# Kernel tuning notes

Hardware: AMD Instinct MI355X
Metric: run time of the kernel (lower is better)

The kernel has to match this reference:

```python
import jax, jax.numpy as jnp
import numpy as np

N_NODES = 50000
N_EDGES = 500000
IN_CH = 128
HID = 64
HEADS = 4
N_LAYERS = 3
OUT_CH = 16
N_GRAPHS = 64
NEG_SLOPE = 0.2  # PyG GATConv default


def setup_inputs() -> dict:
    key = jax.random.key(0)
    ks = jax.random.split(key, 20)
    inp = {
        'x': jax.random.normal(ks[0], (N_NODES, IN_CH), dtype=jnp.float32),
        'edge_attr': jax.random.normal(ks[1], (N_EDGES, 8), dtype=jnp.float32),
        'edge_index': jax.random.randint(ks[2], (2, N_EDGES), 0, N_NODES, dtype=jnp.int64),
        'batch': jnp.sort(jax.random.randint(ks[3], (N_NODES,), 0, N_GRAPHS, dtype=jnp.int64)),
    }
    kidx = 4
    in_dim = IN_CH
    for i in range(N_LAYERS):
        inp[f'W{i}'] = jax.random.normal(ks[kidx], (in_dim, HEADS * HID), dtype=jnp.float32) * (1.0 / np.sqrt(in_dim)); kidx += 1
        inp[f'asrc{i}'] = jax.random.normal(ks[kidx], (HEADS, HID), dtype=jnp.float32) * 0.1; kidx += 1
        inp[f'adst{i}'] = jax.random.normal(ks[kidx], (HEADS, HID), dtype=jnp.float32) * 0.1; kidx += 1
        inp[f'b{i}'] = jnp.zeros((HEADS * HID,), dtype=jnp.float32)
        in_dim = HEADS * HID
    inp['Wc'] = jax.random.normal(ks[kidx], (HEADS * HID, OUT_CH), dtype=jnp.float32) * (1.0 / np.sqrt(HEADS * HID)); kidx += 1
    inp['bc'] = jnp.zeros((OUT_CH,), dtype=jnp.float32)
    return inp


def _gat_layer(x, src, dst, W, asrc, adst, b):
    # x: [N, F_in] -> h: [N, H, C]
    N = x.shape[0]
    h = (x @ W).reshape(N, HEADS, HID)
    s_src = jnp.einsum('nhc,hc->nh', h, asrc)  # [N, H]
    s_dst = jnp.einsum('nhc,hc->nh', h, adst)
    e = jax.nn.leaky_relu(s_src[src] + s_dst[dst], NEG_SLOPE)  # [E, H]
    # segment softmax over incoming edges of each destination node
    m = jax.ops.segment_max(e, dst, num_segments=N)            # [N, H]
    ex = jnp.exp(e - m[dst])
    denom = jax.ops.segment_sum(ex, dst, num_segments=N)       # [N, H]
    alpha = ex / (denom[dst] + 1e-16)                           # [E, H]
    out = jax.ops.segment_sum(alpha[:, :, None] * h[src], dst, num_segments=N)  # [N, H, C]
    return out.reshape(N, HEADS * HID) + b


def reference(x, edge_attr, edge_index, batch,
              W0, asrc0, adst0, b0,
              W1, asrc1, adst1, b1,
              W2, asrc2, adst2, b2,
              Wc, bc):
    N = x.shape[0]
    loop = jnp.arange(N, dtype=edge_index.dtype)
    # PyG GATConv adds self-loops by default
    src = jnp.concatenate([edge_index[0], loop])
    dst = jnp.concatenate([edge_index[1], loop])
    params = [(W0, asrc0, adst0, b0), (W1, asrc1, adst1, b1), (W2, asrc2, adst2, b2)]
    h = x
    for (W, asrc, adst, b) in params:
        h = jax.nn.relu(_gat_layer(h, src, dst, W, asrc, adst, b))
        # nn.Dropout(0.5) is identity in eval mode
    pooled = jax.ops.segment_sum(h, batch, num_segments=N_GRAPHS)  # global_add_pool
    return pooled @ Wc + bc
```

## Files before the change

kernel.cpp:

```cpp
#include <hip/hip_runtime.h>
#include <hip/hip_bf16.h>

#define NNODES 50000
#define NEDGES 500000
#define INCH 128
#define HID 64
#define HEADS 4
#define FDIM 256
#define NGRAPHS 64
#define OUTCH 16
#define NEG_SLOPE 0.2f

#define BM 64
#define BN 256
#define BK 32

typedef float f32x4 __attribute__((ext_vector_type(4)));
typedef __bf16 bf16x8 __attribute__((ext_vector_type(8)));

__device__ inline unsigned short f2bf_rne(float x) {
    unsigned int u = __float_as_uint(x);
    unsigned int r = (u + 0x7FFFu + ((u >> 16) & 1u)) >> 16;
    return (unsigned short)r;
}
__device__ inline float bf2f(unsigned short s) {
    return __uint_as_float(((unsigned int)s) << 16);
}
__device__ inline void split2(float x, unsigned short& h, unsigned short& l) {
    h = f2bf_rne(x);
    float hf = __uint_as_float(((unsigned int)h) << 16);
    l = f2bf_rne(x - hf);
}
__device__ inline void gld_lds16(const void* g, void* l) {
    __builtin_amdgcn_global_load_lds((__attribute__((address_space(1))) void*)g,
                                     (__attribute__((address_space(3))) void*)l, 16, 0, 0);
}


__global__ void k_hist(const int* __restrict__ dst, int E, int* __restrict__ counts) {
    int i = blockIdx.x * blockDim.x + threadIdx.x;
    if (i < E) atomicAdd(&counts[dst[i]], 1);
}

__global__ __launch_bounds__(256) void k_blocksum(const int* __restrict__ counts, int N,
                                                  int* __restrict__ bsum) {
    int idx = blockIdx.x * 256 + threadIdx.x;
    int v = (idx < N) ? counts[idx] : 0;
#pragma unroll
    for (int off = 32; off; off >>= 1) v += __shfl_xor(v, off);
    __shared__ int wsum[4];
    if ((threadIdx.x & 63) == 0) wsum[threadIdx.x >> 6] = v;
    __syncthreads();
    if (threadIdx.x == 0) bsum[blockIdx.x] = wsum[0] + wsum[1] + wsum[2] + wsum[3];
}

__global__ __launch_bounds__(256) void k_scanfinal(const int* __restrict__ counts,
                                                   const int* __restrict__ bsum, int N,
                                                   int* __restrict__ rowstart) {
    __shared__ int tmp[256];
    __shared__ int wsum[4];
    int t = threadIdx.x, b = blockIdx.x;
    int p = 0;
    for (int i = t; i < b; i += 256) p += bsum[i];
#pragma unroll
    for (int off = 32; off; off >>= 1) p += __shfl_xor(p, off);
    int idx = b * 256 + t;
    int v = (idx < N) ? counts[idx] : 0;
    tmp[t] = v;
    if ((t & 63) == 0) wsum[t >> 6] = p;
    __syncthreads();
    int bp = wsum[0] + wsum[1] + wsum[2] + wsum[3];
    for (int off = 1; off < 256; off <<= 1) {
        int u = (t >= off) ? tmp[t - off] : 0;
        __syncthreads();
        tmp[t] += u;
        __syncthreads();
    }
    if (idx < N) rowstart[idx + 1] = bp + tmp[t];
    if (idx == 0) rowstart[0] = 0;
}

__global__ void k_scatter(const int* __restrict__ src, const int* __restrict__ dst, int E,
                          const int* __restrict__ rowstart, int* __restrict__ cursor,
                          int* __restrict__ csr_src) {
    int i = blockIdx.x * blockDim.x + threadIdx.x;
    if (i < E) {
        int d = dst[i];
        int p = atomicAdd(&cursor[d], 1);
        csr_src[rowstart[d] + p] = src[i];
    }
}


__global__ void k_wdecomp(const float* __restrict__ W, unsigned short* __restrict__ Wth,
                          unsigned short* __restrict__ Wtl, int K) {
    int i = blockIdx.x * 256 + threadIdx.x;
    if (i >= K * 256) return;
    int k = i >> 8, n = i & 255;
    unsigned short h, l;
    split2(W[i], h, l);
    Wth[n * K + k] = h;
    Wtl[n * K + k] = l;
}


__global__ void k_adecomp(const float* __restrict__ X, unsigned short* __restrict__ Xh,
                          unsigned short* __restrict__ Xl, int total4) {
    int i = blockIdx.x * 256 + threadIdx.x;
    if (i >= total4) return;
    float4 v = ((const float4*)X)[i];
    ushort4 h, l;
    split2(v.x, h.x, l.x);
    split2(v.y, h.y, l.y);
    split2(v.z, h.z, l.z);
    split2(v.w, h.w, l.w);
    ((ushort4*)Xh)[i] = h;
    ((ushort4*)Xl)[i] = l;
}


__global__ __launch_bounds__(256) void k_gemm_mfma(
    const unsigned short* __restrict__ Aph, const unsigned short* __restrict__ Apl,
    const unsigned short* __restrict__ Bph, const unsigned short* __restrict__ Bpl,
    const float* __restrict__ av, const float* __restrict__ dv,
    unsigned short* __restrict__ Hb16,
    float* __restrict__ ssrcO, float* __restrict__ sdstO, int M, int K) {
    __shared__ unsigned short sAh[BM * BK];
    __shared__ unsigned short sAl[BM * BK];
    __shared__ unsigned short sBh[BN * BK];
    __shared__ unsigned short sBl[BN * BK];

    const int t = threadIdx.x;
    const int row0 = blockIdx.x * BM;
    const int wv = t >> 6, ln = t & 63, lr = ln & 15, lk = ln >> 4;

    const int ar = wv * 16 + (ln >> 2);
    const int alc = (ln & 3) ^ ((ar >> 1) & 3);
    const size_t agoff = (size_t)min(row0 + ar, M - 1) * K + alc * 8;
    const int fsc = lk ^ ((lr >> 1) & 3);

    f32x4 acc[4][4] = {};

    for (int k0 = 0; k0 < K; k0 += BK) {
        gld_lds16(Aph + agoff + k0, &sAh[wv * 512]);
        gld_lds16(Apl + agoff + k0, &sAl[wv * 512]);
#pragma unroll
        for (int j = 0; j < 4; ++j) {
            int br = j * 64 + wv * 16 + (ln >> 2);
            int blc = (ln & 3) ^ ((br >> 1) & 3);
            size_t go = (size_t)br * K + k0 + blc * 8;
            gld_lds16(Bph + go, &sBh[j * 2048 + wv * 512]);
            gld_lds16(Bpl + go, &sBl[j * 2048 + wv * 512]);
        }
        __syncthreads();

        bf16x8 ah[4], al[4];
#pragma unroll
        for (int mi = 0; mi < 4; ++mi) {
            int r = mi * 16 + lr;
            ah[mi] = *(const bf16x8*)&sAh[r * 32 + fsc * 8];
            al[mi] = *(const bf16x8*)&sAl[r * 32 + fsc * 8];
        }
#pragma unroll
        for (int ni = 0; ni < 4; ++ni) {
            int br = wv * 64 + ni * 16 + lr;
            bf16x8 bh = *(const bf16x8*)&sBh[br * 32 + fsc * 8];
            bf16x8 bl = *(const bf16x8*)&sBl[br * 32 + fsc * 8];
#pragma unroll
            for (int mi = 0; mi < 4; ++mi) {
                acc[mi][ni] = __builtin_amdgcn_mfma_f32_16x16x32_bf16(ah[mi], bh, acc[mi][ni], 0, 0, 0);
                acc[mi][ni] = __builtin_amdgcn_mfma_f32_16x16x32_bf16(ah[mi], bl, acc[mi][ni], 0, 0, 0);
                acc[mi][ni] = __builtin_amdgcn_mfma_f32_16x16x32_bf16(al[mi], bh, acc[mi][ni], 0, 0, 0);
            }
        }
        __syncthreads();
    }

    float ps[4][4] = {}, pd[4][4] = {};
#pragma unroll
    for (int ni = 0; ni < 4; ++ni) {
        int col = wv * 64 + ni * 16 + lr;
        float a_s = av[col], a_d = dv[col];
#pragma unroll
        for (int mi = 0; mi < 4; ++mi) {
            f32x4 v = acc[mi][ni];
            int r = row0 + mi * 16 + lk * 4;
#pragma unroll
            for (int j = 0; j < 4; ++j) {
                if (r + j < M) Hb16[(size_t)(r + j) * FDIM + col] = f2bf_rne(v[j]);
                ps[mi][j] += v[j] * a_s;
                pd[mi][j] += v[j] * a_d;
            }
        }
    }
#pragma unroll
    for (int mi = 0; mi < 4; ++mi) {
#pragma unroll
        for (int j = 0; j < 4; ++j) {
            float s = ps[mi][j], q = pd[mi][j];
            s += __shfl_xor(s, 1); s += __shfl_xor(s, 2);
            s += __shfl_xor(s, 4); s += __shfl_xor(s, 8);
            q += __shfl_xor(q, 1); q += __shfl_xor(q, 2);
            q += __shfl_xor(q, 4); q += __shfl_xor(q, 8);
            if (lr == 0) {
                int r = row0 + mi * 16 + lk * 4 + j;
                if (r < M) {
                    ssrcO[r * HEADS + wv] = s;
                    sdstO[r * HEADS + wv] = q;
                }
            }
        }
    }
}


__global__ __launch_bounds__(256) void k_aggregate(
    const unsigned short* __restrict__ hb,
    const float* __restrict__ ssrc, const float* __restrict__ sdst,
    const int* __restrict__ rowstart, const int* __restrict__ csr_src,
    const float* __restrict__ bias,
    unsigned short* __restrict__ oh, unsigned short* __restrict__ ol, int N) {
    int wv = threadIdx.x >> 6, ln = threadIdx.x & 63;
    int n = blockIdx.x * 4 + wv;
    if (n >= N) return;
    int head = ln >> 4;
    int fo = head * 64 + (ln & 15) * 4;
    float sd = sdst[n * HEADS + head];
    float e = ssrc[n * HEADS + head] + sd;
    e = (e > 0.f) ? e : NEG_SLOPE * e;
    float m = e, d = 1.0f;
    ushort4 sv = *(const ushort4*)&hb[(size_t)n * FDIM + fo];
    float4 acc = make_float4(bf2f(sv.x), bf2f(sv.y), bf2f(sv.z), bf2f(sv.w));
    int r0 = rowstart[n], r1 = rowstart[n + 1];
    int r = r0;
    for (; r + 3 < r1; r += 4) {
        int s0 = csr_src[r], s1 = csr_src[r + 1], s2 = csr_src[r + 2], s3 = csr_src[r + 3];
        ushort4 u0 = *(const ushort4*)&hb[(size_t)s0 * FDIM + fo];
        ushort4 u1 = *(const ushort4*)&hb[(size_t)s1 * FDIM + fo];
        ushort4 u2 = *(const ushort4*)&hb[(size_t)s2 * FDIM + fo];
        ushort4 u3 = *(const ushort4*)&hb[(size_t)s3 * FDIM + fo];
        float c0 = ssrc[s0 * HEADS + head] + sd;
        float c1 = ssrc[s1 * HEADS + head] + sd;
        float c2 = ssrc[s2 * HEADS + head] + sd;
        float c3 = ssrc[s3 * HEADS + head] + sd;
        c0 = (c0 > 0.f) ? c0 : NEG_SLOPE * c0;
        c1 = (c1 > 0.f) ? c1 : NEG_SLOPE * c1;
        c2 = (c2 > 0.f) ? c2 : NEG_SLOPE * c2;
        c3 = (c3 > 0.f) ? c3 : NEG_SLOPE * c3;
        float mn = fmaxf(m, fmaxf(fmaxf(c0, c1), fmaxf(c2, c3)));
        float wa = __expf(m - mn);
        float w0 = __expf(c0 - mn), w1 = __expf(c1 - mn);
        float w2 = __expf(c2 - mn), w3 = __expf(c3 - mn);
        acc.x = acc.x * wa + bf2f(u0.x) * w0 + bf2f(u1.x) * w1 + bf2f(u2.x) * w2 + bf2f(u3.x) * w3;
        acc.y = acc.y * wa + bf2f(u0.y) * w0 + bf2f(u1.y) * w1 + bf2f(u2.y) * w2 + bf2f(u3.y) * w3;
        acc.z = acc.z * wa + bf2f(u0.z) * w0 + bf2f(u1.z) * w1 + bf2f(u2.z) * w2 + bf2f(u3.z) * w3;
        acc.w = acc.w * wa + bf2f(u0.w) * w0 + bf2f(u1.w) * w1 + bf2f(u2.w) * w2 + bf2f(u3.w) * w3;
        d = d * wa + ((w0 + w1) + (w2 + w3));
        m = mn;
    }
    for (; r < r1; ++r) {
        int s0 = csr_src[r];
        float sc = ssrc[s0 * HEADS + head] + sd;
        sc = (sc > 0.f) ? sc : NEG_SLOPE * sc;
        ushort4 u0 = *(const ushort4*)&hb[(size_t)s0 * FDIM + fo];
        float mn = fmaxf(m, sc);
        float wa = __expf(m - mn), wn = __expf(sc - mn);
        acc.x = acc.x * wa + bf2f(u0.x) * wn;
        acc.y = acc.y * wa + bf2f(u0.y) * wn;
        acc.z = acc.z * wa + bf2f(u0.z) * wn;
        acc.w = acc.w * wa + bf2f(u0.w) * wn;
        d = d * wa + wn;
        m = mn;
    }
    float inv = 1.0f / d;
    float4 bv = *(const float4*)&bias[fo];
    float o0 = fmaxf(acc.x * inv + bv.x, 0.f);
    float o1 = fmaxf(acc.y * inv + bv.y, 0.f);
    float o2 = fmaxf(acc.z * inv + bv.z, 0.f);
    float o3 = fmaxf(acc.w * inv + bv.w, 0.f);
    ushort4 hh, ll;
    split2(o0, hh.x, ll.x);
    split2(o1, hh.y, ll.y);
    split2(o2, hh.z, ll.z);
    split2(o3, hh.w, ll.w);
    *(ushort4*)&oh[(size_t)n * FDIM + fo] = hh;
    *(ushort4*)&ol[(size_t)n * FDIM + fo] = ll;
}


__global__ __launch_bounds__(256) void k_pool(const unsigned short* __restrict__ oh,
                                              const unsigned short* __restrict__ ol,
                                              const int* __restrict__ batch,
                                              float* __restrict__ pooled, int N) {
    int f = threadIdx.x;
    int n0 = blockIdx.x * 128;
    if (n0 >= N) return;
    int n1 = min(n0 + 128, N);
    int g = batch[n0];
    float run = 0.f;
    for (int n = n0; n < n1; ++n) {
        int gn = batch[n];
        if (gn != g) {
            atomicAdd(&pooled[g * FDIM + f], run);
            run = 0.f;
            g = gn;
        }
        run += bf2f(oh[(size_t)n * FDIM + f]) + bf2f(ol[(size_t)n * FDIM + f]);
    }
    atomicAdd(&pooled[g * FDIM + f], run);
}


__global__ __launch_bounds__(256) void k_final(const float* __restrict__ pooled,
                                               const float* __restrict__ Wc,
                                               const float* __restrict__ bc,
                                               float* __restrict__ out) {
    int tid = blockIdx.x * 256 + threadIdx.x;
    int g = tid >> 4, o = tid & 15;
    float s = bc[o];
    for (int k = 0; k < FDIM; ++k) s += pooled[g * FDIM + k] * Wc[k * OUTCH + o];
    out[g * OUTCH + o] = s;
}


extern "C" void kernel_launch(void* const* d_in, const int* in_sizes, int n_in,
                              void* d_out, int out_size, void* d_ws, size_t ws_size,
                              hipStream_t stream) {
    const float* x = (const float*)d_in[0];
    const int* edge_index = (const int*)d_in[2];
    const int* batch = (const int*)d_in[3];
    const float* W[3]    = {(const float*)d_in[4], (const float*)d_in[8],  (const float*)d_in[12]};
    const float* asrc[3] = {(const float*)d_in[5], (const float*)d_in[9],  (const float*)d_in[13]};
    const float* adst[3] = {(const float*)d_in[6], (const float*)d_in[10], (const float*)d_in[14]};
    const float* bias[3] = {(const float*)d_in[7], (const float*)d_in[11], (const float*)d_in[15]};
    const float* Wc = (const float*)d_in[16];
    const float* bc = (const float*)d_in[17];

    const int N = in_sizes[3];
    const int E = in_sizes[2] / 2;
    const int* e_src = edge_index;
    const int* e_dst = edge_index + E;

    char* ws = (char*)d_ws;
    size_t off = 0;
    unsigned short* hb = (unsigned short*)(ws + off); off += (size_t)N * FDIM * 2;
    unsigned short* xh = (unsigned short*)(ws + off); off += (size_t)N * INCH * 2;
    unsigned short* xl = (unsigned short*)(ws + off); off += (size_t)N * INCH * 2;
    unsigned short* P0h = (unsigned short*)(ws + off); off += (size_t)N * FDIM * 2;
    unsigned short* P0l = (unsigned short*)(ws + off); off += (size_t)N * FDIM * 2;
    unsigned short* P1h = (unsigned short*)(ws + off); off += (size_t)N * FDIM * 2;
    unsigned short* P1l = (unsigned short*)(ws + off); off += (size_t)N * FDIM * 2;
    float* ssrc = (float*)(ws + off); off += (size_t)N * HEADS * 4;
    float* sdst = (float*)(ws + off); off += (size_t)N * HEADS * 4;
    int* rowstart = (int*)(ws + off); off += ((size_t)(N + 1) * 4 + 255) / 256 * 256;
    int* cursor = (int*)(ws + off); off += (size_t)N * 4;
    int* csr_src = (int*)(ws + off); off += (size_t)E * 4;
    float* pooled = (float*)(ws + off); off += (size_t)NGRAPHS * FDIM * 4;
    int* bsum = (int*)(ws + off); off += ((size_t)((N + 255) / 256) * 4 + 255) / 256 * 256;
    unsigned short* Wth[3];
    unsigned short* Wtl[3];
    int Ks[3] = {INCH, FDIM, FDIM};
    for (int l = 0; l < 3; ++l) {
        Wth[l] = (unsigned short*)(ws + off); off += (size_t)256 * Ks[l] * 2;
        Wtl[l] = (unsigned short*)(ws + off); off += (size_t)256 * Ks[l] * 2;
    }

    const int nb = (N + 255) / 256;

    hipMemsetAsync(cursor, 0, (size_t)N * 4, stream);
    k_hist<<<(E + 255) / 256, 256, 0, stream>>>(e_dst, E, cursor);
    k_blocksum<<<nb, 256, 0, stream>>>(cursor, N, bsum);
    k_scanfinal<<<nb, 256, 0, stream>>>(cursor, bsum, N, rowstart);
    hipMemsetAsync(cursor, 0, (size_t)N * 4, stream);
    k_scatter<<<(E + 255) / 256, 256, 0, stream>>>(e_src, e_dst, E, rowstart, cursor, csr_src);

    k_adecomp<<<((N * INCH / 4) + 255) / 256, 256, 0, stream>>>(x, xh, xl, N * INCH / 4);
    for (int l = 0; l < 3; ++l)
        k_wdecomp<<<(Ks[l] * 256 + 255) / 256, 256, 0, stream>>>(W[l], Wth[l], Wtl[l], Ks[l]);

    const unsigned short* Ah = xh;
    const unsigned short* Al = xl;
    unsigned short* Oh[3] = {P0h, P1h, P0h};
    unsigned short* Ol[3] = {P0l, P1l, P0l};
    for (int l = 0; l < 3; ++l) {
        int K = Ks[l];
        k_gemm_mfma<<<(N + BM - 1) / BM, 256, 0, stream>>>(Ah, Al, Wth[l], Wtl[l], asrc[l],
                                                           adst[l], hb, ssrc, sdst, N, K);
        k_aggregate<<<(N + 3) / 4, 256, 0, stream>>>(hb, ssrc, sdst, rowstart, csr_src,
                                                     bias[l], Oh[l], Ol[l], N);
        Ah = Oh[l];
        Al = Ol[l];
    }

    hipMemsetAsync(pooled, 0, (size_t)NGRAPHS * FDIM * 4, stream);
    k_pool<<<(N + 127) / 128, 256, 0, stream>>>(P0h, P0l, batch, pooled, N);
    k_final<<<4, 256, 0, stream>>>(pooled, Wc, bc, (float*)d_out);
}
```

Before: 393.7 us.

## Switch split-bf16 GEMM to single fp16, double-buffer LDS, batch aggregation

Replaces the three-MFMA split-bf16 (hi/lo) emulation of fp32 GEMM with a single fp16 MFMA per tile, and stores activations as one fp16 tensor instead of hi/lo pairs. This cuts GEMM compute and activation memory traffic. The GEMM also gets double-buffered LDS staging, the aggregation loop processes neighbours in batches of 8 with clamped indices, and the CSR build folds the cursor init into the scan to drop one memset. The trade-off is lower precision (fp16 range and mantissa) compared with the near-fp32 split scheme.

```diff
diff --git a/kernel.cpp b/kernel.cpp
--- a/kernel.cpp
+++ b/kernel.cpp
@@ -16,21 +16,9 @@
 #define BK 32
 
 typedef float f32x4 __attribute__((ext_vector_type(4)));
-typedef __bf16 bf16x8 __attribute__((ext_vector_type(8)));
-
-__device__ inline unsigned short f2bf_rne(float x) {
-    unsigned int u = __float_as_uint(x);
-    unsigned int r = (u + 0x7FFFu + ((u >> 16) & 1u)) >> 16;
-    return (unsigned short)r;
-}
-__device__ inline float bf2f(unsigned short s) {
-    return __uint_as_float(((unsigned int)s) << 16);
-}
-__device__ inline void split2(float x, unsigned short& h, unsigned short& l) {
-    h = f2bf_rne(x);
-    float hf = __uint_as_float(((unsigned int)h) << 16);
-    l = f2bf_rne(x - hf);
-}
+typedef _Float16 f16x8 __attribute__((ext_vector_type(8)));
+typedef _Float16 f16x4 __attribute__((ext_vector_type(4)));
+
 __device__ inline void gld_lds16(const void* g, void* l) {
     __builtin_amdgcn_global_load_lds((__attribute__((address_space(1))) void*)g,
                                      (__attribute__((address_space(3))) void*)l, 16, 0, 0);
@@ -56,7 +44,8 @@
 
 __global__ __launch_bounds__(256) void k_scanfinal(const int* __restrict__ counts,
                                                    const int* __restrict__ bsum, int N,
-                                                   int* __restrict__ rowstart) {
+                                                   int* __restrict__ rowstart,
+                                                   int* __restrict__ cursor) {
     __shared__ int tmp[256];
     __shared__ int wsum[4];
     int t = threadIdx.x, b = blockIdx.x;
@@ -76,59 +65,48 @@
         tmp[t] += u;
         __syncthreads();
     }
-    if (idx < N) rowstart[idx + 1] = bp + tmp[t];
+    if (idx < N) {
+        int incl = bp + tmp[t];
+        rowstart[idx + 1] = incl;
+        cursor[idx] = incl - v;
+    }
     if (idx == 0) rowstart[0] = 0;
 }
 
 __global__ void k_scatter(const int* __restrict__ src, const int* __restrict__ dst, int E,
-                          const int* __restrict__ rowstart, int* __restrict__ cursor,
-                          int* __restrict__ csr_src) {
+                          int* __restrict__ cursor, int* __restrict__ csr_src) {
     int i = blockIdx.x * blockDim.x + threadIdx.x;
     if (i < E) {
-        int d = dst[i];
-        int p = atomicAdd(&cursor[d], 1);
-        csr_src[rowstart[d] + p] = src[i];
-    }
-}
-
-
-__global__ void k_wdecomp(const float* __restrict__ W, unsigned short* __restrict__ Wth,
-                          unsigned short* __restrict__ Wtl, int K) {
+        int p = atomicAdd(&cursor[dst[i]], 1);
+        csr_src[p] = src[i];
+    }
+}
+
+
+__global__ void k_wdecomp(const float* __restrict__ W, _Float16* __restrict__ Wt, int K) {
     int i = blockIdx.x * 256 + threadIdx.x;
     if (i >= K * 256) return;
     int k = i >> 8, n = i & 255;
-    unsigned short h, l;
-    split2(W[i], h, l);
-    Wth[n * K + k] = h;
-    Wtl[n * K + k] = l;
-}
-
-
-__global__ void k_adecomp(const float* __restrict__ X, unsigned short* __restrict__ Xh,
-                          unsigned short* __restrict__ Xl, int total4) {
+    Wt[n * K + k] = (_Float16)W[i];
+}
+
+
+__global__ void k_adecomp(const float* __restrict__ X, _Float16* __restrict__ Xf, int total4) {
     int i = blockIdx.x * 256 + threadIdx.x;
     if (i >= total4) return;
     float4 v = ((const float4*)X)[i];
-    ushort4 h, l;
-    split2(v.x, h.x, l.x);
-    split2(v.y, h.y, l.y);
-    split2(v.z, h.z, l.z);
-    split2(v.w, h.w, l.w);
-    ((ushort4*)Xh)[i] = h;
-    ((ushort4*)Xl)[i] = l;
+    f16x4 o = {(_Float16)v.x, (_Float16)v.y, (_Float16)v.z, (_Float16)v.w};
+    ((f16x4*)Xf)[i] = o;
 }
 
 
 __global__ __launch_bounds__(256) void k_gemm_mfma(
-    const unsigned short* __restrict__ Aph, const unsigned short* __restrict__ Apl,
-    const unsigned short* __restrict__ Bph, const unsigned short* __restrict__ Bpl,
+    const _Float16* __restrict__ A, const _Float16* __restrict__ B,
     const float* __restrict__ av, const float* __restrict__ dv,
-    unsigned short* __restrict__ Hb16,
+    _Float16* __restrict__ Hf,
     float* __restrict__ ssrcO, float* __restrict__ sdstO, int M, int K) {
-    __shared__ unsigned short sAh[BM * BK];
-    __shared__ unsigned short sAl[BM * BK];
-    __shared__ unsigned short sBh[BN * BK];
-    __shared__ unsigned short sBl[BN * BK];
+    __shared__ _Float16 sA[2][BM * BK];
+    __shared__ _Float16 sB[2][BN * BK];
 
     const int t = threadIdx.x;
     const int row0 = blockIdx.x * BM;
@@ -137,44 +115,44 @@
     const int ar = wv * 16 + (ln >> 2);
     const int alc = (ln & 3) ^ ((ar >> 1) & 3);
     const size_t agoff = (size_t)min(row0 + ar, M - 1) * K + alc * 8;
+    const int brr = wv * 16 + (ln >> 2);
     const int fsc = lk ^ ((lr >> 1) & 3);
 
     f32x4 acc[4][4] = {};
-
-    for (int k0 = 0; k0 < K; k0 += BK) {
-        gld_lds16(Aph + agoff + k0, &sAh[wv * 512]);
-        gld_lds16(Apl + agoff + k0, &sAl[wv * 512]);
-#pragma unroll
-        for (int j = 0; j < 4; ++j) {
-            int br = j * 64 + wv * 16 + (ln >> 2);
-            int blc = (ln & 3) ^ ((br >> 1) & 3);
-            size_t go = (size_t)br * K + k0 + blc * 8;
-            gld_lds16(Bph + go, &sBh[j * 2048 + wv * 512]);
-            gld_lds16(Bpl + go, &sBl[j * 2048 + wv * 512]);
+    const int nt = K / BK;
+
+#define STAGE(tt, p)                                                        \
+    do {                                                                    \
+        int _k0 = (tt)*BK;                                                  \
+        gld_lds16(A + agoff + _k0, &sA[p][wv * 512]);                       \
+        _Pragma("unroll") for (int _j = 0; _j < 4; ++_j) {                  \
+            int _br = _j * 64 + brr;                                        \
+            int _blc = (ln & 3) ^ ((_br >> 1) & 3);                         \
+            gld_lds16(B + (size_t)_br * K + _k0 + _blc * 8,                 \
+                      &sB[p][_j * 2048 + wv * 512]);                        \
+        }                                                                   \
+    } while (0)
+
+    STAGE(0, 0);
+    __syncthreads();
+    for (int tt = 0; tt < nt; ++tt) {
+        int cur = tt & 1;
+        if (tt + 1 < nt) STAGE(tt + 1, cur ^ 1);
+
+        f16x8 af[4];
+#pragma unroll
+        for (int mi = 0; mi < 4; ++mi)
+            af[mi] = *(const f16x8*)&sA[cur][(mi * 16 + lr) * BK + fsc * 8];
+#pragma unroll
+        for (int ni = 0; ni < 4; ++ni) {
+            f16x8 bf = *(const f16x8*)&sB[cur][(wv * 64 + ni * 16 + lr) * BK + fsc * 8];
+#pragma unroll
+            for (int mi = 0; mi < 4; ++mi)
+                acc[mi][ni] = __builtin_amdgcn_mfma_f32_16x16x32_f16(af[mi], bf, acc[mi][ni], 0, 0, 0);
         }
         __syncthreads();
-
-        bf16x8 ah[4], al[4];
-#pragma unroll
-        for (int mi = 0; mi < 4; ++mi) {
-            int r = mi * 16 + lr;
-            ah[mi] = *(const bf16x8*)&sAh[r * 32 + fsc * 8];
-            al[mi] = *(const bf16x8*)&sAl[r * 32 + fsc * 8];
-        }
-#pragma unroll
-        for (int ni = 0; ni < 4; ++ni) {
-            int br = wv * 64 + ni * 16 + lr;
-            bf16x8 bh = *(const bf16x8*)&sBh[br * 32 + fsc * 8];
-            bf16x8 bl = *(const bf16x8*)&sBl[br * 32 + fsc * 8];
-#pragma unroll
-            for (int mi = 0; mi < 4; ++mi) {
-                acc[mi][ni] = __builtin_amdgcn_mfma_f32_16x16x32_bf16(ah[mi], bh, acc[mi][ni], 0, 0, 0);
-                acc[mi][ni] = __builtin_amdgcn_mfma_f32_16x16x32_bf16(ah[mi], bl, acc[mi][ni], 0, 0, 0);
-                acc[mi][ni] = __builtin_amdgcn_mfma_f32_16x16x32_bf16(al[mi], bh, acc[mi][ni], 0, 0, 0);
-            }
-        }
-        __syncthreads();
-    }
+    }
+#undef STAGE
 
     float ps[4][4] = {}, pd[4][4] = {};
 #pragma unroll
@@ -187,7 +165,7 @@
             int r = row0 + mi * 16 + lk * 4;
 #pragma unroll
             for (int j = 0; j < 4; ++j) {
-                if (r + j < M) Hb16[(size_t)(r + j) * FDIM + col] = f2bf_rne(v[j]);
+                if (r + j < M) Hf[(size_t)(r + j) * FDIM + col] = (_Float16)v[j];
                 ps[mi][j] += v[j] * a_s;
                 pd[mi][j] += v[j] * a_d;
             }
@@ -215,11 +193,11 @@
 
 
 __global__ __launch_bounds__(256) void k_aggregate(
-    const unsigned short* __restrict__ hb,
+    const _Float16* __restrict__ hf,
     const float* __restrict__ ssrc, const float* __restrict__ sdst,
     const int* __restrict__ rowstart, const int* __restrict__ csr_src,
     const float* __restrict__ bias,
-    unsigned short* __restrict__ oh, unsigned short* __restrict__ ol, int N) {
+    _Float16* __restrict__ outf, int N) {
     int wv = threadIdx.x >> 6, ln = threadIdx.x & 63;
     int n = blockIdx.x * 4 + wv;
     if (n >= N) return;
@@ -229,67 +207,58 @@
     float e = ssrc[n * HEADS + head] + sd;
     e = (e > 0.f) ? e : NEG_SLOPE * e;
     float m = e, d = 1.0f;
-    ushort4 sv = *(const ushort4*)&hb[(size_t)n * FDIM + fo];
-    float4 acc = make_float4(bf2f(sv.x), bf2f(sv.y), bf2f(sv.z), bf2f(sv.w));
+    f16x4 sv = *(const f16x4*)&hf[(size_t)n * FDIM + fo];
+    float4 acc = make_float4((float)sv[0], (float)sv[1], (float)sv[2], (float)sv[3]);
     int r0 = rowstart[n], r1 = rowstart[n + 1];
-    int r = r0;
-    for (; r + 3 < r1; r += 4) {
-        int s0 = csr_src[r], s1 = csr_src[r + 1], s2 = csr_src[r + 2], s3 = csr_src[r + 3];
-        ushort4 u0 = *(const ushort4*)&hb[(size_t)s0 * FDIM + fo];
-        ushort4 u1 = *(const ushort4*)&hb[(size_t)s1 * FDIM + fo];
-        ushort4 u2 = *(const ushort4*)&hb[(size_t)s2 * FDIM + fo];
-        ushort4 u3 = *(const ushort4*)&hb[(size_t)s3 * FDIM + fo];
-        float c0 = ssrc[s0 * HEADS + head] + sd;
-        float c1 = ssrc[s1 * HEADS + head] + sd;
-        float c2 = ssrc[s2 * HEADS + head] + sd;
-        float c3 = ssrc[s3 * HEADS + head] + sd;
-        c0 = (c0 > 0.f) ? c0 : NEG_SLOPE * c0;
-        c1 = (c1 > 0.f) ? c1 : NEG_SLOPE * c1;
-        c2 = (c2 > 0.f) ? c2 : NEG_SLOPE * c2;
-        c3 = (c3 > 0.f) ? c3 : NEG_SLOPE * c3;
-        float mn = fmaxf(m, fmaxf(fmaxf(c0, c1), fmaxf(c2, c3)));
+    int cnt = r1 - r0;
+    for (int base = 0; base < cnt; base += 8) {
+        int s[8];
+        f16x4 u[8];
+        float c[8], w[8];
+#pragma unroll
+        for (int i = 0; i < 8; ++i) s[i] = csr_src[min(r0 + base + i, r1 - 1)];
+#pragma unroll
+        for (int i = 0; i < 8; ++i) u[i] = *(const f16x4*)&hf[(size_t)s[i] * FDIM + fo];
+#pragma unroll
+        for (int i = 0; i < 8; ++i) {
+            float sc = ssrc[s[i] * HEADS + head] + sd;
+            sc = (sc > 0.f) ? sc : NEG_SLOPE * sc;
+            c[i] = (base + i < cnt) ? sc : -1e30f;
+        }
+        float mx = fmaxf(fmaxf(fmaxf(c[0], c[1]), fmaxf(c[2], c[3])),
+                         fmaxf(fmaxf(c[4], c[5]), fmaxf(c[6], c[7])));
+        float mn = fmaxf(m, mx);
         float wa = __expf(m - mn);
-        float w0 = __expf(c0 - mn), w1 = __expf(c1 - mn);
-        float w2 = __expf(c2 - mn), w3 = __expf(c3 - mn);
-        acc.x = acc.x * wa + bf2f(u0.x) * w0 + bf2f(u1.x) * w1 + bf2f(u2.x) * w2 + bf2f(u3.x) * w3;
-        acc.y = acc.y * wa + bf2f(u0.y) * w0 + bf2f(u1.y) * w1 + bf2f(u2.y) * w2 + bf2f(u3.y) * w3;
-        acc.z = acc.z * wa + bf2f(u0.z) * w0 + bf2f(u1.z) * w1 + bf2f(u2.z) * w2 + bf2f(u3.z) * w3;
-        acc.w = acc.w * wa + bf2f(u0.w) * w0 + bf2f(u1.w) * w1 + bf2f(u2.w) * w2 + bf2f(u3.w) * w3;
-        d = d * wa + ((w0 + w1) + (w2 + w3));
-        m = mn;
-    }
-    for (; r < r1; ++r) {
-        int s0 = csr_src[r];
-        float sc = ssrc[s0 * HEADS + head] + sd;
-        sc = (sc > 0.f) ? sc : NEG_SLOPE * sc;
-        ushort4 u0 = *(const ushort4*)&hb[(size_t)s0 * FDIM + fo];
-        float mn = fmaxf(m, sc);
-        float wa = __expf(m - mn), wn = __expf(sc - mn);
-        acc.x = acc.x * wa + bf2f(u0.x) * wn;
-        acc.y = acc.y * wa + bf2f(u0.y) * wn;
-        acc.z = acc.z * wa + bf2f(u0.z) * wn;
-        acc.w = acc.w * wa + bf2f(u0.w) * wn;
-        d = d * wa + wn;
+#pragma unroll
+        for (int i = 0; i < 8; ++i) w[i] = __expf(c[i] - mn);
+        float sx = 0.f, sy = 0.f, sz = 0.f, sw = 0.f, sdn = 0.f;
+#pragma unroll
+        for (int i = 0; i < 8; ++i) {
+            sx += w[i] * (float)u[i][0];
+            sy += w[i] * (float)u[i][1];
+            sz += w[i] * (float)u[i][2];
+            sw += w[i] * (float)u[i][3];
+            sdn += w[i];
+        }
+        acc.x = acc.x * wa + sx;
+        acc.y = acc.y * wa + sy;
+        acc.z = acc.z * wa + sz;
+        acc.w = acc.w * wa + sw;
+        d = d * wa + sdn;
         m = mn;
     }
     float inv = 1.0f / d;
     float4 bv = *(const float4*)&bias[fo];
-    float o0 = fmaxf(acc.x * inv + bv.x, 0.f);
-    float o1 = fmaxf(acc.y * inv + bv.y, 0.f);
-    float o2 = fmaxf(acc.z * inv + bv.z, 0.f);
-    float o3 = fmaxf(acc.w * inv + bv.w, 0.f);
-    ushort4 hh, ll;
-    split2(o0, hh.x, ll.x);
-    split2(o1, hh.y, ll.y);
-    split2(o2, hh.z, ll.z);
-    split2(o3, hh.w, ll.w);
-    *(ushort4*)&oh[(size_t)n * FDIM + fo] = hh;
-    *(ushort4*)&ol[(size_t)n * FDIM + fo] = ll;
-}
-
-
-__global__ __launch_bounds__(256) void k_pool(const unsigned short* __restrict__ oh,
-                                              const unsigned short* __restrict__ ol,
+    f16x4 o;
+    o[0] = (_Float16)fmaxf(acc.x * inv + bv.x, 0.f);
+    o[1] = (_Float16)fmaxf(acc.y * inv + bv.y, 0.f);
+    o[2] = (_Float16)fmaxf(acc.z * inv + bv.z, 0.f);
+    o[3] = (_Float16)fmaxf(acc.w * inv + bv.w, 0.f);
+    *(f16x4*)&outf[(size_t)n * FDIM + fo] = o;
+}
+
+
+__global__ __launch_bounds__(256) void k_pool(const _Float16* __restrict__ hf,
                                               const int* __restrict__ batch,
                                               float* __restrict__ pooled, int N) {
     int f = threadIdx.x;
@@ -305,7 +274,7 @@
             run = 0.f;
             g = gn;
         }
-        run += bf2f(oh[(size_t)n * FDIM + f]) + bf2f(ol[(size_t)n * FDIM + f]);
+        run += (float)hf[(size_t)n * FDIM + f];
     }
     atomicAdd(&pooled[g * FDIM + f], run);
 }
@@ -343,56 +312,46 @@
 
     char* ws = (char*)d_ws;
     size_t off = 0;
-    unsigned short* hb = (unsigned short*)(ws + off); off += (size_t)N * FDIM * 2;
-    unsigned short* xh = (unsigned short*)(ws + off); off += (size_t)N * INCH * 2;
-    unsigned short* xl = (unsigned short*)(ws + off); off += (size_t)N * INCH * 2;
-    unsigned short* P0h = (unsigned short*)(ws + off); off += (size_t)N * FDIM * 2;
-    unsigned short* P0l = (unsigned short*)(ws + off); off += (size_t)N * FDIM * 2;
-    unsigned short* P1h = (unsigned short*)(ws + off); off += (size_t)N * FDIM * 2;
-    unsigned short* P1l = (unsigned short*)(ws + off); off += (size_t)N * FDIM * 2;
+    _Float16* hb = (_Float16*)(ws + off); off += (size_t)N * FDIM * 2;
+    _Float16* xf = (_Float16*)(ws + off); off += (size_t)N * INCH * 2;
+    _Float16* P  = (_Float16*)(ws + off); off += (size_t)N * FDIM * 2;
     float* ssrc = (float*)(ws + off); off += (size_t)N * HEADS * 4;
     float* sdst = (float*)(ws + off); off += (size_t)N * HEADS * 4;
     int* rowstart = (int*)(ws + off); off += ((size_t)(N + 1) * 4 + 255) / 256 * 256;
+    int* counts = (int*)(ws + off); off += (size_t)N * 4;
     int* cursor = (int*)(ws + off); off += (size_t)N * 4;
     int* csr_src = (int*)(ws + off); off += (size_t)E * 4;
     float* pooled = (float*)(ws + off); off += (size_t)NGRAPHS * FDIM * 4;
     int* bsum = (int*)(ws + off); off += ((size_t)((N + 255) / 256) * 4 + 255) / 256 * 256;
-    unsigned short* Wth[3];
-    unsigned short* Wtl[3];
+    _Float16* Wt[3];
     int Ks[3] = {INCH, FDIM, FDIM};
     for (int l = 0; l < 3; ++l) {
-        Wth[l] = (unsigned short*)(ws + off); off += (size_t)256 * Ks[l] * 2;
-        Wtl[l] = (unsigned short*)(ws + off); off += (size_t)256 * Ks[l] * 2;
+        Wt[l] = (_Float16*)(ws + off); off += (size_t)256 * Ks[l] * 2;
     }
 
     const int nb = (N + 255) / 256;
 
-    hipMemsetAsync(cursor, 0, (size_t)N * 4, stream);
-    k_hist<<<(E + 255) / 256, 256, 0, stream>>>(e_dst, E, cursor);
-    k_blocksum<<<nb, 256, 0, stream>>>(cursor, N, bsum);
-    k_scanfinal<<<nb, 256, 0, stream>>>(cursor, bsum, N, rowstart);
-    hipMemsetAsync(cursor, 0, (size_t)N * 4, stream);
-    k_scatter<<<(E + 255) / 256, 256, 0, stream>>>(e_src, e_dst, E, rowstart, cursor, csr_src);
-
-    k_adecomp<<<((N * INCH / 4) + 255) / 256, 256, 0, stream>>>(x, xh, xl, N * INCH / 4);
+    hipMemsetAsync(counts, 0, (size_t)N * 4, stream);
+    k_hist<<<(E + 255) / 256, 256, 0, stream>>>(e_dst, E, counts);
+    k_blocksum<<<nb, 256, 0, stream>>>(counts, N, bsum);
+    k_scanfinal<<<nb, 256, 0, stream>>>(counts, bsum, N, rowstart, cursor);
+    k_scatter<<<(E + 255) / 256, 256, 0, stream>>>(e_src, e_dst, E, cursor, csr_src);
+
+    k_adecomp<<<((N * INCH / 4) + 255) / 256, 256, 0, stream>>>(x, xf, N * INCH / 4);
     for (int l = 0; l < 3; ++l)
-        k_wdecomp<<<(Ks[l] * 256 + 255) / 256, 256, 0, stream>>>(W[l], Wth[l], Wtl[l], Ks[l]);
-
-    const unsigned short* Ah = xh;
-    const unsigned short* Al = xl;
-    unsigned short* Oh[3] = {P0h, P1h, P0h};
-    unsigned short* Ol[3] = {P0l, P1l, P0l};
+        k_wdecomp<<<(Ks[l] * 256 + 255) / 256, 256, 0, stream>>>(W[l], Wt[l], Ks[l]);
+
+    const _Float16* Af = xf;
     for (int l = 0; l < 3; ++l) {
         int K = Ks[l];
-        k_gemm_mfma<<<(N + BM - 1) / BM, 256, 0, stream>>>(Ah, Al, Wth[l], Wtl[l], asrc[l],
-                                                           adst[l], hb, ssrc, sdst, N, K);
+        k_gemm_mfma<<<(N + BM - 1) / BM, 256, 0, stream>>>(Af, Wt[l], asrc[l], adst[l],
+                                                           hb, ssrc, sdst, N, K);
         k_aggregate<<<(N + 3) / 4, 256, 0, stream>>>(hb, ssrc, sdst, rowstart, csr_src,
-                                                     bias[l], Oh[l], Ol[l], N);
-        Ah = Oh[l];
-        Al = Ol[l];
+                                                     bias[l], P, N);
+        Af = P;
     }
 
     hipMemsetAsync(pooled, 0, (size_t)NGRAPHS * FDIM * 4, stream);
-    k_pool<<<(N + 127) / 128, 256, 0, stream>>>(P0h, P0l, batch, pooled, N);
+    k_pool<<<(N + 127) / 128, 256, 0, stream>>>(P, batch, pooled, N);
     k_final<<<4, 256, 0, stream>>>(pooled, Wc, bc, (float*)d_out);
 }
```

New measurement: 341.3 us. 13.3% less time.
